# Performance work log

Measured on AMD Instinct MI355X. Metric: run time of the kernel, lower is better.

Reference implementation:

```python
import jax, jax.numpy as jnp
import numpy as np
from jax import lax

B, S, D = 8, 1024, 128

def setup_inputs() -> dict:
    key = jax.random.key(0)
    ks = jax.random.split(key, 6)
    scale = 1.0 / np.sqrt(D)
    return {
        "x": jax.random.normal(ks[0], (B, S, D), dtype=jnp.float32),
        "Wk": jax.random.normal(ks[1], (D, D), dtype=jnp.float32) * scale,
        "Wv": jax.random.normal(ks[2], (D, D), dtype=jnp.float32) * scale,
        "Wq": jax.random.normal(ks[3], (D, D), dtype=jnp.float32) * scale,
        "Wg": jax.random.normal(ks[4], (D, 3), dtype=jnp.float32) * scale,
        "bg": jnp.zeros((3,), dtype=jnp.float32),
    }

def reference(x, Wk, Wv, Wq, Wg, bg):
    b, s, d = x.shape
    k = x @ Wk  # [b,s,d]
    v = x @ Wv
    q = x @ Wq
    gates = jax.nn.sigmoid(x @ Wg + bg)  # [b,s,3]
    alpha, eta, theta = gates[..., 0], gates[..., 1], gates[..., 2]  # [b,s]

    M0 = jnp.zeros((b, d, d), dtype=x.dtype)
    S0 = jnp.zeros((b, d, d), dtype=x.dtype)

    # time-major scan inputs
    xs = (jnp.swapaxes(k, 0, 1), jnp.swapaxes(v, 0, 1), jnp.swapaxes(q, 0, 1),
          jnp.swapaxes(alpha, 0, 1), jnp.swapaxes(eta, 0, 1), jnp.swapaxes(theta, 0, 1))

    def scan_fn(carry, inp):
        M_prev, S_prev = carry
        kt, vt, qt, at, et, tt = inp  # kt/vt/qt: [b,d]; at/et/tt: [b]
        # NOTE: original einsum 'bd,bdd->bd' takes the DIAGONAL of M (faithful)
        diagM = jnp.einsum('bdd->bd', M_prev)  # [b,d]
        yt = qt * diagM
        pred = kt * diagM
        error = pred - vt
        grad = kt[:, :, None] * error[:, None, :]  # outer product [b,d,d]
        S_new = et[:, None, None] * S_prev - tt[:, None, None] * grad
        M_new = (1.0 - at[:, None, None]) * M_prev + S_new
        return (M_new, S_new), yt

    (M_final, S_final), outputs = lax.scan(scan_fn, (M0, S0), xs)
    outputs = jnp.swapaxes(outputs, 0, 1)  # [b,s,d]
    return (outputs, (M_final, S_final))
```

## Files before the change

### kernel.cpp

```cpp
#include <hip/hip_runtime.h>
#include <math.h>

#define NB 8
#define NS 1024
#define ND 128
#define NC 64
#define NL 16

#define OFF_K  0u
#define OFF_Q  1048576u
#define OFF_V  2097152u
#define OFF_E  3145728u
#define OFF_GA 4194304u
#define OFF_GE 4202496u
#define OFF_GT 4210688u
#define OFF_W  4218880u
#define OFF_C  4227072u
#define OFF_P  4235264u

#define PL_A00 (OFF_P)
#define PL_A01 (OFF_P +  65536u)
#define PL_A10 (OFF_P + 131072u)
#define PL_A11 (OFF_P + 196608u)
#define PL_B0  (OFF_P + 262144u)
#define PL_B1  (OFF_P + 327680u)
#define PL_MST (OFF_P + 393216u)
#define PL_SST (OFF_P + 458752u)
#define PL_WCA (OFF_P + 524288u)
#define PL_WCB (OFF_P + 524800u)
#define PL_WCD (OFF_P + 525312u)
#define PL_WRQ (OFF_P + 525824u)
#define PL_WRP (OFF_P + 526336u)
#define PL_WRA (OFF_P + 526848u)
#define OFF_WT (OFF_P + 532480u)
#define WT_LO  49152u

typedef short bf16x8 __attribute__((ext_vector_type(8)));
typedef float f32x4  __attribute__((ext_vector_type(4)));

static __device__ __forceinline__ unsigned short f2bf(float f) {
    unsigned u = __builtin_bit_cast(unsigned, f);
    unsigned r = (u + 0x7FFFu + ((u >> 16) & 1u)) >> 16;
    return (unsigned short)r;
}
static __device__ __forceinline__ float bf2f(unsigned short h) {
    unsigned u = ((unsigned)h) << 16;
    return __builtin_bit_cast(float, u);
}
static __device__ __forceinline__ void split2(float a, float b,
                                              unsigned& hi, unsigned& lo) {
    unsigned short ah = f2bf(a), bh = f2bf(b);
    float ar = a - bf2f(ah), br = b - bf2f(bh);
    hi = (unsigned)ah | ((unsigned)bh << 16);
    lo = (unsigned)f2bf(ar) | ((unsigned)f2bf(br) << 16);
}

__global__ __launch_bounds__(256) void wtprep_kernel(
    const float* __restrict__ Wk, const float* __restrict__ Wv,
    const float* __restrict__ Wq, unsigned short* __restrict__ wtg,
    float* __restrict__ outMS)
{
    const int m    = blockIdx.x >> 4;
    const int cgrp = blockIdx.x & 15;
    const int tid  = threadIdx.x;
    const int cl   = tid >> 5;
    const int h    = tid & 31;
    const int c    = cgrp * 8 + cl;
    const float* W = (m == 0) ? Wk : (m == 1) ? Wv : Wq;

    float f[4];
#pragma unroll
    for (int i = 0; i < 4; ++i)
        f[i] = W[(h * 4 + i) * ND + c];
    uint2 hi, lo;
    split2(f[0], f[1], hi.x, lo.x);
    split2(f[2], f[3], hi.y, lo.y);
    const unsigned base = (unsigned)m * 16384u + (unsigned)c * 128u + (unsigned)h * 4u;
    *(uint2*)&wtg[base]         = hi;
    *(uint2*)&wtg[WT_LO + base] = lo;

    const int gidx = blockIdx.x * 256 + tid;
    const float4 z = {0.f, 0.f, 0.f, 0.f};
#pragma unroll
    for (int l = 0; l < 6; ++l) {
        int i4 = gidx + l * 12288;
        if (i4 < 65536) ((float4*)outMS)[i4] = z;
    }
}

__global__ __launch_bounds__(256) void proj_mfma(
    const float* __restrict__ x, const unsigned short* __restrict__ wtg,
    const float* __restrict__ Wg, const float* __restrict__ bg,
    float* __restrict__ Kb, float* __restrict__ Vb, float* __restrict__ Qb,
    float* __restrict__ ga, float* __restrict__ ge, float* __restrict__ gt)
{
    __shared__ unsigned short xs_hi[32 * 136];
    __shared__ unsigned short xs_lo[32 * 136];
    __shared__ unsigned short wt_hi[64 * 136];
    __shared__ unsigned short wt_lo[64 * 136];

    const int tid  = threadIdx.x;
    const int bid  = blockIdx.x;
    const int m    = bid >> 9;
    const int rt   = (bid >> 1) & 255;
    const int ch   = bid & 1;
    const int row0 = rt * 32;

    const float4* x4 = (const float4*)x;
#pragma unroll
    for (int l = 0; l < 4; ++l) {
        int idx = tid + l * 256;
        int r = idx >> 5, kq = idx & 31;
        float4 f = x4[(row0 + r) * 32 + kq];
        uint2 hi, lo;
        split2(f.x, f.y, hi.x, lo.x);
        split2(f.z, f.w, hi.y, lo.y);
        *(uint2*)&xs_hi[r * 136 + kq * 4] = hi;
        *(uint2*)&xs_lo[r * 136 + kq * 4] = lo;
    }
    const uint4* wh4 = (const uint4*)(wtg + m * 16384 + ch * 64 * 128);
    const uint4* wl4 = (const uint4*)(wtg + WT_LO + m * 16384 + ch * 64 * 128);
#pragma unroll
    for (int l = 0; l < 4; ++l) {
        int idx = tid + l * 256;
        int c = idx >> 4, u = idx & 15;
        *(uint4*)&wt_hi[c * 136 + u * 8] = wh4[c * 16 + u];
        *(uint4*)&wt_lo[c * 136 + u * 8] = wl4[c * 16 + u];
    }
    __syncthreads();

    const int wid  = tid >> 6;
    const int lane = tid & 63;
    const int rg   = wid >> 1;
    const int cg   = wid & 1;
    const int lrow = rg * 16 + (lane & 15);
    const int quad = lane >> 4;

    f32x4 acc[2];
    acc[0] = (f32x4){0.f, 0.f, 0.f, 0.f};
    acc[1] = (f32x4){0.f, 0.f, 0.f, 0.f};

#pragma unroll
    for (int kk = 0; kk < 4; ++kk) {
        bf16x8 ah = *(const bf16x8*)&xs_hi[lrow * 136 + kk * 32 + quad * 8];
        bf16x8 al = *(const bf16x8*)&xs_lo[lrow * 136 + kk * 32 + quad * 8];
#pragma unroll
        for (int ct = 0; ct < 2; ++ct) {
            int cl = cg * 32 + ct * 16 + (lane & 15);
            bf16x8 bh = *(const bf16x8*)&wt_hi[cl * 136 + kk * 32 + quad * 8];
            bf16x8 bl = *(const bf16x8*)&wt_lo[cl * 136 + kk * 32 + quad * 8];
            acc[ct] = __builtin_amdgcn_mfma_f32_16x16x32_bf16(ah, bh, acc[ct], 0, 0, 0);
            acc[ct] = __builtin_amdgcn_mfma_f32_16x16x32_bf16(ah, bl, acc[ct], 0, 0, 0);
            acc[ct] = __builtin_amdgcn_mfma_f32_16x16x32_bf16(al, bh, acc[ct], 0, 0, 0);
        }
    }

    float* dst = (m == 0) ? Kb : (m == 1) ? Vb : Qb;
#pragma unroll
    for (int ct = 0; ct < 2; ++ct) {
        int ocol = ch * 64 + cg * 32 + ct * 16 + (lane & 15);
#pragma unroll
        for (int r4 = 0; r4 < 4; ++r4) {
            int orow = row0 + rg * 16 + quad * 4 + r4;
            dst[orow * ND + ocol] = acc[ct][r4];
        }
    }

    if (m == 0 && ch == 0 && tid < 192) {
        int p = tid >> 1;
        int h = tid & 1;
        int r = p / 3, j = p % 3;
        const float4* x4r = (const float4*)(x + (row0 + r) * ND + h * 64);
        float z = 0.f;
#pragma unroll
        for (int i4 = 0; i4 < 16; ++i4) {
            float4 f = x4r[i4];
            int i = h * 64 + i4 * 4;
            z = fmaf(f.x, Wg[(i    ) * 3 + j], z);
            z = fmaf(f.y, Wg[(i + 1) * 3 + j], z);
            z = fmaf(f.z, Wg[(i + 2) * 3 + j], z);
            z = fmaf(f.w, Wg[(i + 3) * 3 + j], z);
        }
        z += __shfl_xor(z, 1);
        if (h == 0) {
            z += bg[j];
            float gate = 1.0f / (1.0f + expf(-z));
            float* gd = (j == 0) ? ga : (j == 1) ? ge : gt;
            gd[row0 + r] = gate;
        }
    }
}

__global__ __launch_bounds__(128) void scan_phase1(
    const float* __restrict__ Kb, const float* __restrict__ Vb,
    const float* __restrict__ ga, const float* __restrict__ ge,
    const float* __restrict__ gt, float* __restrict__ ws)
{
    __shared__ float la[NL], le[NL], lt[NL];
    const int tid = threadIdx.x;
    const int b   = blockIdx.x >> 6;
    const int c   = blockIdx.x & 63;
    const int t0  = c * NL;
    const int g0  = b * NS + t0;

    if (tid < 16)       la[tid]      = ga[g0 + tid];
    else if (tid < 32)  le[tid - 16] = ge[g0 + tid - 16];
    else if (tid < 48)  lt[tid - 32] = gt[g0 + tid - 32];
    __syncthreads();

    const int d = tid;
    float A00 = 1.f, A01 = 0.f, A10 = 0.f, A11 = 1.f, B0 = 0.f, B1 = 0.f;
    int base = g0 * ND + d;
#pragma unroll
    for (int t = 0; t < NL; ++t) {
        float k = Kb[base], v = Vb[base];
        float a = la[t], e = le[t], th = lt[t];
        float tk = th * k;
        float gg = -tk * k;
        float h  = tk * v;
        float p  = (1.0f - a) + gg;
        float u0 = e * A10;
        float u1 = e * A11;
        float u2 = fmaf(e, B1, h);
        float n00 = fmaf(p, A00, u0), n10 = fmaf(gg, A00, u0);
        float n01 = fmaf(p, A01, u1), n11 = fmaf(gg, A01, u1);
        float nb0 = fmaf(p, B0, u2),  nb1 = fmaf(gg, B0, u2);
        A00 = n00; A01 = n01; A10 = n10; A11 = n11; B0 = nb0; B1 = nb1;
        base += ND;
    }
    const int pidx = (b * NC + c) * ND + d;
    ws[PL_A00 + pidx] = A00;
    ws[PL_A01 + pidx] = A01;
    ws[PL_A10 + pidx] = A10;
    ws[PL_A11 + pidx] = A11;
    ws[PL_B0  + pidx] = B0;
    ws[PL_B1  + pidx] = B1;

    if (tid == 0) {
        float al = 1.f, be = 1.f, de = 0.f;
#pragma unroll
        for (int t = NL - 1; t >= 0; --t) {
            float e1 = le[t];
            float o1 = 1.0f - la[t];
            de = fmaf(e1, de, o1 * be);
            al *= e1;
            be *= o1;
        }
        ws[PL_WCA + b * NC + c] = al;
        ws[PL_WCB + b * NC + c] = be;
        ws[PL_WCD + b * NC + c] = de;
    }
}

__global__ __launch_bounds__(64) void scan_phase2(float* __restrict__ ws)
{
    const int tid = threadIdx.x;
    if (blockIdx.x < 16) {
        const int b = blockIdx.x >> 1;
        const int d = (blockIdx.x & 1) * 64 + tid;
        float m = 0.f, s = 0.f;
        int idx = (b * NC) * ND + d;
#pragma unroll 4
        for (int c = 0; c < NC; ++c) {
            ws[PL_MST + idx] = m;
            ws[PL_SST + idx] = s;
            float A00 = ws[PL_A00 + idx], A01 = ws[PL_A01 + idx];
            float A10 = ws[PL_A10 + idx], A11 = ws[PL_A11 + idx];
            float B0  = ws[PL_B0  + idx], B1  = ws[PL_B1  + idx];
            float nm = fmaf(A00, m, fmaf(A01, s, B0));
            float ns = fmaf(A10, m, fmaf(A11, s, B1));
            m = nm; s = ns;
            idx += ND;
        }
    } else if (tid < 8) {
        const int b = tid;
        float Qp = 1.f, P = 1.f, A = 1.f;
        for (int c = NC - 1; c >= 0; --c) {
            ws[PL_WRQ + b * NC + c] = Qp;
            ws[PL_WRP + b * NC + c] = P;
            ws[PL_WRA + b * NC + c] = A;
            float al = ws[PL_WCA + b * NC + c];
            float be = ws[PL_WCB + b * NC + c];
            float de = ws[PL_WCD + b * NC + c];
            float nA = fmaf(al, A, de * P);
            Qp *= al; P *= be; A = nA;
        }
    }
}

__global__ __launch_bounds__(128) void scan_phase3(
    const float* __restrict__ Kb, const float* __restrict__ Vb,
    const float* __restrict__ Qb,
    const float* __restrict__ ga, const float* __restrict__ ge,
    const float* __restrict__ gt,
    float* __restrict__ out, float* __restrict__ errb,
    float* __restrict__ wb,  float* __restrict__ cb,
    float* __restrict__ ws)
{
    __shared__ float la[NL], le[NL], lt[NL];
    const int tid = threadIdx.x;
    const int b   = blockIdx.x >> 6;
    const int c   = blockIdx.x & 63;
    const int t0  = c * NL;
    const int g0  = b * NS + t0;

    if (tid < 16)       la[tid]      = ga[g0 + tid];
    else if (tid < 32)  le[tid - 16] = ge[g0 + tid - 16];
    else if (tid < 48)  lt[tid - 32] = gt[g0 + tid - 32];
    __syncthreads();

    const int d = tid;
    const int pidx = (b * NC + c) * ND + d;
    float m = ws[PL_MST + pidx];
    float s = ws[PL_SST + pidx];
    int base = g0 * ND + d;
#pragma unroll
    for (int t = 0; t < NL; ++t) {
        float k = Kb[base], v = Vb[base], q = Qb[base];
        float a = la[t], e = le[t], th = lt[t];
        float err = fmaf(k, m, -v);
        out[base]  = q * m;
        errb[base] = err;
        float tk = th * k;
        float u  = fmaf(-(tk * k), m, tk * v);
        s = fmaf(e, s, u);
        m = fmaf(1.0f - a, m, s);
        base += ND;
    }

    if (tid == 0) {
        float Qp = ws[PL_WRQ + b * NC + c];
        float P  = ws[PL_WRP + b * NC + c];
        float A  = ws[PL_WRA + b * NC + c];
#pragma unroll
        for (int t = NL - 1; t >= 0; --t) {
            wb[g0 + t] = -lt[t] * Qp;
            cb[g0 + t] = -lt[t] * A;
            float e1 = le[t];
            float o1 = 1.0f - la[t];
            Qp *= e1;
            P  *= o1;
            A   = fmaf(e1, A, P);
        }
    }
}

__global__ __launch_bounds__(256) void finalgemm_kernel(
    const float* __restrict__ Kb, const float* __restrict__ errb,
    const float* __restrict__ wb, const float* __restrict__ cb,
    float* __restrict__ outMS)
{
    __shared__ float ks[64 * 16];
    __shared__ float wcs[64 * 2];
    const int tid = threadIdx.x;
    const int bid = blockIdx.x;
    const int b   = bid >> 7;
    const int tc  = (bid >> 3) & 15;
    const int rg  = bid & 7;
    const int bt0 = b * NS + tc * 64;

    {
        int tl = tid >> 2, r4 = tid & 3;
        *(float4*)&ks[tl * 16 + r4 * 4] =
            *(const float4*)&Kb[(bt0 + tl) * ND + rg * 16 + r4 * 4];
    }
    if (tid < 64) {
        wcs[tid * 2]     = wb[bt0 + tid];
        wcs[tid * 2 + 1] = cb[bt0 + tid];
    }
    __syncthreads();

    const int j = tid & 127;
    const int h = tid >> 7;
    float accM[8], accS[8];
#pragma unroll
    for (int i = 0; i < 8; ++i) { accM[i] = 0.f; accS[i] = 0.f; }

    int ebase = bt0 * ND + j;
#pragma unroll 4
    for (int t = 0; t < 64; ++t) {
        float ej = errb[ebase];
        float2 wc = *(const float2*)&wcs[t * 2];
        float wej = wc.x * ej, cej = wc.y * ej;
        float4 k0 = *(const float4*)&ks[t * 16 + h * 8];
        float4 k1 = *(const float4*)&ks[t * 16 + h * 8 + 4];
        accS[0] = fmaf(k0.x, wej, accS[0]); accM[0] = fmaf(k0.x, cej, accM[0]);
        accS[1] = fmaf(k0.y, wej, accS[1]); accM[1] = fmaf(k0.y, cej, accM[1]);
        accS[2] = fmaf(k0.z, wej, accS[2]); accM[2] = fmaf(k0.z, cej, accM[2]);
        accS[3] = fmaf(k0.w, wej, accS[3]); accM[3] = fmaf(k0.w, cej, accM[3]);
        accS[4] = fmaf(k1.x, wej, accS[4]); accM[4] = fmaf(k1.x, cej, accM[4]);
        accS[5] = fmaf(k1.y, wej, accS[5]); accM[5] = fmaf(k1.y, cej, accM[5]);
        accS[6] = fmaf(k1.z, wej, accS[6]); accM[6] = fmaf(k1.z, cej, accM[6]);
        accS[7] = fmaf(k1.w, wej, accS[7]); accM[7] = fmaf(k1.w, cej, accM[7]);
        ebase += ND;
    }

    const int robase = rg * 16 + h * 8;
#pragma unroll
    for (int i = 0; i < 8; ++i) {
        int off = b * (ND * ND) + (robase + i) * ND + j;
        atomicAdd(&outMS[off], accM[i]);
        atomicAdd(&outMS[131072u + off], accS[i]);
    }
}

extern "C" void kernel_launch(void* const* d_in, const int* in_sizes, int n_in,
                              void* d_out, int out_size, void* d_ws, size_t ws_size,
                              hipStream_t stream) {
    const float* x  = (const float*)d_in[0];
    const float* Wk = (const float*)d_in[1];
    const float* Wv = (const float*)d_in[2];
    const float* Wq = (const float*)d_in[3];
    const float* Wg = (const float*)d_in[4];
    const float* bg = (const float*)d_in[5];
    float* out = (float*)d_out;
    float* ws  = (float*)d_ws;

    float* Kb  = ws + OFF_K;
    float* Qb  = ws + OFF_Q;
    float* Vb  = ws + OFF_V;
    float* Eb  = ws + OFF_E;
    float* ga  = ws + OFF_GA;
    float* ge  = ws + OFF_GE;
    float* gt  = ws + OFF_GT;
    float* wbf = ws + OFF_W;
    float* cbf = ws + OFF_C;
    float* outMS = out + 1048576u;
    unsigned short* wtg = (unsigned short*)(ws + OFF_WT);

    wtprep_kernel<<<48, 256, 0, stream>>>(Wk, Wv, Wq, wtg, outMS);
    proj_mfma<<<1536, 256, 0, stream>>>(x, wtg, Wg, bg,
                                        Kb, Vb, Qb, ga, ge, gt);
    scan_phase1<<<NB * NC, 128, 0, stream>>>(Kb, Vb, ga, ge, gt, ws);
    scan_phase2<<<17, 64, 0, stream>>>(ws);
    scan_phase3<<<NB * NC, 128, 0, stream>>>(Kb, Vb, Qb, ga, ge, gt,
                                             out, Eb, wbf, cbf, ws);
    finalgemm_kernel<<<1024, 256, 0, stream>>>(Kb, Eb, wbf, cbf, outMS);
}
```

Measured before the change: 117.9 us.

## Fold chunk-prefix scan into phase3, removing the serial phase2 kernel

After: 116.8 us. About the same (-0.9%).

```diff
diff --git a/kernel.cpp b/kernel.cpp
--- a/kernel.cpp
+++ b/kernel.cpp
@@ -24,14 +24,9 @@
 #define PL_A11 (OFF_P + 196608u)
 #define PL_B0  (OFF_P + 262144u)
 #define PL_B1  (OFF_P + 327680u)
-#define PL_MST (OFF_P + 393216u)
-#define PL_SST (OFF_P + 458752u)
 #define PL_WCA (OFF_P + 524288u)
 #define PL_WCB (OFF_P + 524800u)
 #define PL_WCD (OFF_P + 525312u)
-#define PL_WRQ (OFF_P + 525824u)
-#define PL_WRP (OFF_P + 526336u)
-#define PL_WRA (OFF_P + 526848u)
 #define OFF_WT (OFF_P + 532480u)
 #define WT_LO  49152u
 
@@ -252,43 +247,7 @@
     }
 }
 
-__global__ __launch_bounds__(64) void scan_phase2(float* __restrict__ ws)
-{
-    const int tid = threadIdx.x;
-    if (blockIdx.x < 16) {
-        const int b = blockIdx.x >> 1;
-        const int d = (blockIdx.x & 1) * 64 + tid;
-        float m = 0.f, s = 0.f;
-        int idx = (b * NC) * ND + d;
-#pragma unroll 4
-        for (int c = 0; c < NC; ++c) {
-            ws[PL_MST + idx] = m;
-            ws[PL_SST + idx] = s;
-            float A00 = ws[PL_A00 + idx], A01 = ws[PL_A01 + idx];
-            float A10 = ws[PL_A10 + idx], A11 = ws[PL_A11 + idx];
-            float B0  = ws[PL_B0  + idx], B1  = ws[PL_B1  + idx];
-            float nm = fmaf(A00, m, fmaf(A01, s, B0));
-            float ns = fmaf(A10, m, fmaf(A11, s, B1));
-            m = nm; s = ns;
-            idx += ND;
-        }
-    } else if (tid < 8) {
-        const int b = tid;
-        float Qp = 1.f, P = 1.f, A = 1.f;
-        for (int c = NC - 1; c >= 0; --c) {
-            ws[PL_WRQ + b * NC + c] = Qp;
-            ws[PL_WRP + b * NC + c] = P;
-            ws[PL_WRA + b * NC + c] = A;
-            float al = ws[PL_WCA + b * NC + c];
-            float be = ws[PL_WCB + b * NC + c];
-            float de = ws[PL_WCD + b * NC + c];
-            float nA = fmaf(al, A, de * P);
-            Qp *= al; P *= be; A = nA;
-        }
-    }
-}
-
-__global__ __launch_bounds__(128) void scan_phase3(
+__global__ __launch_bounds__(128) void scan_phase3b(
     const float* __restrict__ Kb, const float* __restrict__ Vb,
     const float* __restrict__ Qb,
     const float* __restrict__ ga, const float* __restrict__ ge,
@@ -300,7 +259,7 @@
     __shared__ float la[NL], le[NL], lt[NL];
     const int tid = threadIdx.x;
     const int b   = blockIdx.x >> 6;
-    const int c   = blockIdx.x & 63;
+    const int c   = 63 - (blockIdx.x & 63);
     const int t0  = c * NL;
     const int g0  = b * NS + t0;
 
@@ -310,9 +269,22 @@
     __syncthreads();
 
     const int d = tid;
-    const int pidx = (b * NC + c) * ND + d;
-    float m = ws[PL_MST + pidx];
-    float s = ws[PL_SST + pidx];
+
+    float m = 0.f, s = 0.f;
+    {
+        int idx = (b * NC) * ND + d;
+#pragma unroll 4
+        for (int cc = 0; cc < c; ++cc) {
+            float A00 = ws[PL_A00 + idx], A01 = ws[PL_A01 + idx];
+            float A10 = ws[PL_A10 + idx], A11 = ws[PL_A11 + idx];
+            float B0  = ws[PL_B0  + idx], B1  = ws[PL_B1  + idx];
+            float nm = fmaf(A00, m, fmaf(A01, s, B0));
+            float ns = fmaf(A10, m, fmaf(A11, s, B1));
+            m = nm; s = ns;
+            idx += ND;
+        }
+    }
+
     int base = g0 * ND + d;
 #pragma unroll
     for (int t = 0; t < NL; ++t) {
@@ -329,9 +301,14 @@
     }
 
     if (tid == 0) {
-        float Qp = ws[PL_WRQ + b * NC + c];
-        float P  = ws[PL_WRP + b * NC + c];
-        float A  = ws[PL_WRA + b * NC + c];
+        float Qp = 1.f, P = 1.f, A = 1.f;
+        for (int cc = NC - 1; cc > c; --cc) {
+            float al = ws[PL_WCA + b * NC + cc];
+            float be = ws[PL_WCB + b * NC + cc];
+            float de = ws[PL_WCD + b * NC + cc];
+            float nA = fmaf(al, A, de * P);
+            Qp *= al; P *= be; A = nA;
+        }
 #pragma unroll
         for (int t = NL - 1; t >= 0; --t) {
             wb[g0 + t] = -lt[t] * Qp;
@@ -432,8 +409,7 @@
     proj_mfma<<<1536, 256, 0, stream>>>(x, wtg, Wg, bg,
                                         Kb, Vb, Qb, ga, ge, gt);
     scan_phase1<<<NB * NC, 128, 0, stream>>>(Kb, Vb, ga, ge, gt, ws);
-    scan_phase2<<<17, 64, 0, stream>>>(ws);
-    scan_phase3<<<NB * NC, 128, 0, stream>>>(Kb, Vb, Qb, ga, ge, gt,
-                                             out, Eb, wbf, cbf, ws);
+    scan_phase3b<<<NB * NC, 128, 0, stream>>>(Kb, Vb, Qb, ga, ge, gt,
+                                              out, Eb, wbf, cbf, ws);
     finalgemm_kernel<<<1024, 256, 0, stream>>>(Kb, Eb, wbf, cbf, outMS);
 }
```
